# Performance work log

Measured on AMD Instinct MI355X. Metric: run time of the kernel, lower is better.

The kernel has to match this reference:

```python
import jax, jax.numpy as jnp
import numpy as np

HIDDEN = 2048
INTER = 768
NUM_EXPERTS = 32
TOP_K = 4
NUM_TOKENS = 2048


def setup_inputs() -> dict:
    key = jax.random.key(0)
    ks = jax.random.split(key, 5)
    scale = 0.02
    x = jax.random.normal(ks[0], (NUM_TOKENS, HIDDEN), dtype=jnp.float32)
    w_router = jax.random.normal(ks[1], (HIDDEN, NUM_EXPERTS), dtype=jnp.float32) * scale
    w_gate = jax.random.normal(ks[2], (NUM_EXPERTS, HIDDEN, INTER), dtype=jnp.float32) * scale
    w_up = jax.random.normal(ks[3], (NUM_EXPERTS, HIDDEN, INTER), dtype=jnp.float32) * scale
    w_down = jax.random.normal(ks[4], (NUM_EXPERTS, INTER, HIDDEN), dtype=jnp.float32) * scale
    return {"hidden_states": x, "w_router": w_router, "w_gate": w_gate,
            "w_up": w_up, "w_down": w_down}


def reference(hidden_states, w_router, w_gate, w_up, w_down):
    x = hidden_states  # [T, H]
    T = x.shape[0]
    # Router: softmax over experts (in input dtype), top-k, renormalize.
    router_logits = x @ w_router                      # [T, E]
    routing_weights = jax.nn.softmax(router_logits, axis=-1)
    top_w, top_idx = jax.lax.top_k(routing_weights, TOP_K)  # [T, K]
    top_w = top_w / jnp.sum(top_w, axis=-1, keepdims=True)   # norm_topk_prob
    # Dense combine weights: combine[t, e] = routing weight if expert e selected
    # for token t, else 0.  (top-k indices are unique per token.)
    combine = jnp.zeros((T, NUM_EXPERTS), dtype=x.dtype)
    combine = combine.at[jnp.arange(T)[:, None], top_idx].add(top_w)  # [T, E]

    # Scan over experts: each step computes one expert's SwiGLU MLP on all
    # tokens and accumulates it weighted by its combine weight (tokens with
    # zero weight contribute nothing, matching the gather/scatter original).
    def body(acc, expert):
        wg, wu, wd, cw = expert  # [H,I], [H,I], [I,H], [T]
        h = jax.nn.silu(x @ wg) * (x @ wu)   # [T, I]
        return acc + (h @ wd) * cw[:, None], None

    out, _ = jax.lax.scan(body, jnp.zeros_like(x),
                          (w_gate, w_up, w_down, combine.T))
    return out
```

## Files before the change

kernel.cpp:

```cpp
#include <hip/hip_runtime.h>

#define T_TOK 2048
#define HID   2048
#define INTER 768
#define NE    32
#define NSLOT 8192
#define MAXT  96

typedef short bf16x8 __attribute__((ext_vector_type(8)));
typedef float f32x4  __attribute__((ext_vector_type(4)));

__device__ __forceinline__ unsigned short f2b(float f){
  unsigned u = __builtin_bit_cast(unsigned, f);
  u += 0x7fffu + ((u >> 16) & 1u);
  return (unsigned short)(u >> 16);
}
__device__ __forceinline__ unsigned pk2(float a, float b){
  return (unsigned)f2b(a) | ((unsigned)f2b(b) << 16);
}

#define XB_OFF    0ul
#define HBUF_OFF  8388608ul
#define TKW_OFF   20971520ul
#define TKI_OFF   21004288ul
#define ROWS_OFF  21037056ul
#define WTS_OFF   21069824ul
#define OFFS_OFF  21102592ul
#define LOGIT_OFF 21102848ul
#define CNT_OFF   21364992ul
#define FILL_OFF  21365120ul
#define TLIST_OFF 21365248ul
#define T2S_OFF   21365760ul
#define HB2_OFF   21398528ul
#define WS_NEED   (HB2_OFF + 67108864ul)
#define ZERO_OFF  21102848ul
#define ZERO_SZ   (262144ul + 128ul + 128ul)

__global__ void convert_x_kernel(const float* __restrict__ x, ushort* __restrict__ xb){
  int i = (blockIdx.x * 256 + threadIdx.x) * 8;
  float4 a = *(const float4*)(x + i);
  float4 b = *(const float4*)(x + i + 4);
  uint4 o;
  o.x = pk2(a.x, a.y);
  o.y = pk2(a.z, a.w);
  o.z = pk2(b.x, b.y);
  o.w = pk2(b.z, b.w);
  *(uint4*)(xb + i) = o;
}

__global__ void router_gemm(const float* __restrict__ x, const float* __restrict__ wr,
                            float* __restrict__ logits){
  const int tt = blockIdx.x;
  const int kb = blockIdx.y;
  __shared__ float xs[64 * 64];
  __shared__ float wsm[64 * 32];
  const int tid = threadIdx.x;
  const int r = tid >> 5, e = tid & 31;
  float acc[8];
#pragma unroll
  for (int i = 0; i < 8; i++) acc[i] = 0.0f;

  for (int sub = 0; sub < 4; ++sub){
    const int k0 = kb * 256 + sub * 64;
    __syncthreads();
#pragma unroll
    for (int j = 0; j < 4; j++){
      int f4 = tid + j * 256;
      int row = f4 >> 4, c4 = f4 & 15;
      float4 v = *(const float4*)(x + (size_t)(tt * 64 + row) * HID + k0 + c4 * 4);
      *(float4*)(xs + row * 64 + c4 * 4) = v;
    }
#pragma unroll
    for (int j = 0; j < 2; j++){
      int f4 = tid + j * 256;
      int row = f4 >> 3, c4 = f4 & 7;
      float4 v = *(const float4*)(wr + (size_t)(k0 + row) * NE + c4 * 4);
      *(float4*)(wsm + row * NE + c4 * 4) = v;
    }
    __syncthreads();
    for (int kk = 0; kk < 64; kk++){
      float wv = wsm[kk * NE + e];
#pragma unroll
      for (int i = 0; i < 8; i++) acc[i] += xs[(r + i * 8) * 64 + kk] * wv;
    }
  }
#pragma unroll
  for (int i = 0; i < 8; i++)
    atomicAdd(&logits[(size_t)(tt * 64 + r + i * 8) * NE + e], acc[i]);
}

__global__ void topk_kernel(const float* __restrict__ logits, float* __restrict__ topk_w,
                            int* __restrict__ topk_i, int* __restrict__ counts){
  int t = blockIdx.x * blockDim.x + threadIdx.x;
  if (t >= T_TOK) return;
  float l[32];
  const float4* lp = (const float4*)(logits + (size_t)t * NE);
#pragma unroll
  for (int i = 0; i < 8; i++){
    float4 v = lp[i];
    l[i*4+0] = v.x; l[i*4+1] = v.y; l[i*4+2] = v.z; l[i*4+3] = v.w;
  }
  float m = l[0];
#pragma unroll
  for (int i = 1; i < 32; i++) m = fmaxf(m, l[i]);
#pragma unroll
  for (int i = 0; i < 32; i++) l[i] = __expf(l[i] - m);
  float wsel[4]; int isel[4];
#pragma unroll
  for (int k = 0; k < 4; k++){
    float best = l[0]; int bi = 0;
#pragma unroll
    for (int i = 1; i < 32; i++){ if (l[i] > best){ best = l[i]; bi = i; } }
    wsel[k] = best; isel[k] = bi; l[bi] = -1.0f;
  }
  float s4 = wsel[0] + wsel[1] + wsel[2] + wsel[3];
  float inv = 1.0f / s4;
#pragma unroll
  for (int k = 0; k < 4; k++){
    topk_w[t * 4 + k] = wsel[k] * inv;
    topk_i[t * 4 + k] = isel[k];
    atomicAdd(&counts[isel[k]], 1);
  }
}

__global__ void prefix_kernel(const int* __restrict__ counts, int* __restrict__ offsets,
                              int* __restrict__ tlist){
  if (threadIdx.x == 0){
    int a = 0; offsets[0] = 0; int nt_ = 0;
    for (int e = 0; e < NE; e++){
      int c = counts[e];
      for (int m = 0; m * 128 < c && nt_ < MAXT; m++) tlist[nt_++] = e | (m << 16);
      a += c; offsets[e + 1] = a;
    }
    for (; nt_ < MAXT; nt_++) tlist[nt_] = -1;
  }
}

__global__ void scatter_kernel(const int* __restrict__ topk_i, const float* __restrict__ topk_w,
                               const int* __restrict__ offsets, int* __restrict__ fill,
                               int* __restrict__ rows, float* __restrict__ wts,
                               int* __restrict__ t2s){
  int gid = blockIdx.x * 256 + threadIdx.x;
  int t = gid >> 2;
  int e = topk_i[gid];
  int pos = atomicAdd(&fill[e], 1);
  int s = offsets[e] + pos;
  rows[s] = t;
  wts[s] = topk_w[gid];
  t2s[gid] = s;
}

#define NT_GU 32
__global__ __launch_bounds__(512) void gateup_kernel(
    const ushort* __restrict__ xb, const float* __restrict__ wg,
    const float* __restrict__ wu, const int* __restrict__ rows,
    const float* __restrict__ wts, const int* __restrict__ counts,
    const int* __restrict__ offsets, const int* __restrict__ tlist,
    ushort* __restrict__ hbuf)
{
  const int w = tlist[blockIdx.y];
  if (w < 0) return;
  const int e = w & 0xffff, mt = w >> 16;
  const int nt = blockIdx.x;
  const int cnt = counts[e];
  const int off = offsets[e];
  const int n0 = nt * 64;

  __shared__ __align__(16) ushort lds[2 * 16384];

  const int tid = threadIdx.x;

  const int ra = tid >> 2, quad = tid & 3;
  const int srow = mt * 128 + ra;
  const int slotA = off + (srow < cnt ? srow : 0);
  const int tokA = rows[slotA];
  const ushort* agp = xb + (size_t)tokA * HID;
  const int q0 = quad * 2, q1 = q0 + 1;
  const int axk = ra & 7;
  const int adst0 = ra * 64 + (q0 ^ axk) * 8;
  const int adst1 = ra * 64 + (q1 ^ axk) * 8;

  const int bn = tid & 63, kg = tid >> 6;
  const size_t wofs = (size_t)e * (HID * INTER) + n0 + bn;
  const float* wgp = wg + wofs;
  const float* wup = wu + wofs;
  const int bdst = bn * 64 + (kg ^ (bn & 7)) * 8;

  const int lane = tid & 63, wv = tid >> 6;
  const int wm = wv >> 1, wn = wv & 1;
  const int fr = lane & 15, ko = lane >> 4;
  const int fxk = fr & 7;

  f32x4 accg[2][2], accu[2][2];
#pragma unroll
  for (int i = 0; i < 2; i++)
#pragma unroll
    for (int j = 0; j < 2; j++){ accg[i][j] = (f32x4)(0.0f); accu[i][j] = (f32x4)(0.0f); }

  uint4 A0a, A0b, A1a, A1b;
  float G0[8], U0[8], G1[8], U1[8];

  auto loadSet = [&](int k0, uint4 &aa, uint4 &ab, float *g, float *u){
    aa = *(const uint4*)(agp + k0 + q0 * 8);
    ab = *(const uint4*)(agp + k0 + q1 * 8);
    const float* pg_ = wgp + (size_t)(k0 + kg * 8) * INTER;
    const float* pu_ = wup + (size_t)(k0 + kg * 8) * INTER;
#pragma unroll
    for (int kk = 0; kk < 8; kk++){ g[kk] = pg_[(size_t)kk * INTER]; u[kk] = pu_[(size_t)kk * INTER]; }
  };
  auto writeSet = [&](int base, uint4 aa, uint4 ab, const float *g, const float *u){
    ushort* dA = lds + base;
    *(uint4*)(dA + adst0) = aa;
    *(uint4*)(dA + adst1) = ab;
    uint4 pg, pu;
    pg.x = pk2(g[0], g[1]); pg.y = pk2(g[2], g[3]);
    pg.z = pk2(g[4], g[5]); pg.w = pk2(g[6], g[7]);
    pu.x = pk2(u[0], u[1]); pu.y = pk2(u[2], u[3]);
    pu.z = pk2(u[4], u[5]); pu.w = pk2(u[6], u[7]);
    *(uint4*)(dA + 8192 + bdst) = pg;
    *(uint4*)(dA + 12288 + bdst) = pu;
  };
  auto computeTile = [&](int base){
    const ushort* A  = lds + base;
    const ushort* BG = lds + base + 8192;
    const ushort* BU = lds + base + 12288;
#pragma unroll
    for (int kk = 0; kk < 2; kk++){
      const int bsel = ((kk * 4 + ko) ^ fxk) * 8;
      bf16x8 a[2], bg2[2], bu2[2];
#pragma unroll
      for (int mf = 0; mf < 2; mf++)
        a[mf] = *(const bf16x8*)(A + (wm * 32 + mf * 16 + fr) * 64 + bsel);
#pragma unroll
      for (int nf = 0; nf < 2; nf++){
        bg2[nf] = *(const bf16x8*)(BG + (wn * 32 + nf * 16 + fr) * 64 + bsel);
        bu2[nf] = *(const bf16x8*)(BU + (wn * 32 + nf * 16 + fr) * 64 + bsel);
      }
#pragma unroll
      for (int mf = 0; mf < 2; mf++)
#pragma unroll
        for (int nf = 0; nf < 2; nf++){
          accg[mf][nf] = __builtin_amdgcn_mfma_f32_16x16x32_bf16(a[mf], bg2[nf], accg[mf][nf], 0, 0, 0);
          accu[mf][nf] = __builtin_amdgcn_mfma_f32_16x16x32_bf16(a[mf], bu2[nf], accu[mf][nf], 0, 0, 0);
        }
    }
  };

  loadSet(0,  A0a, A0b, G0, U0);
  loadSet(64, A1a, A1b, G1, U1);
  writeSet(0, A0a, A0b, G0, U0);
  __syncthreads();

  for (int t = 0; t < NT_GU; t += 2){
    if (t + 2 < NT_GU) loadSet((t + 2) * 64, A0a, A0b, G0, U0);
    computeTile(0);
    writeSet(16384, A1a, A1b, G1, U1);
    __syncthreads();
    if (t + 3 < NT_GU) loadSet((t + 3) * 64, A1a, A1b, G1, U1);
    computeTile(16384);
    if (t + 2 < NT_GU) writeSet(0, A0a, A0b, G0, U0);
    __syncthreads();
  }

#pragma unroll
  for (int mf = 0; mf < 2; mf++)
#pragma unroll
    for (int j = 0; j < 4; j++){
      int rl = wm * 32 + mf * 16 + ko * 4 + j;
      int gr = mt * 128 + rl;
      if (gr < cnt){
        float w2 = wts[off + gr];
        size_t robase = (size_t)(off + gr) * INTER + n0;
#pragma unroll
        for (int nf = 0; nf < 2; nf++){
          float g = accg[mf][nf][j], u = accu[mf][nf][j];
          float h = (g / (1.0f + __expf(-g))) * u * w2;
          hbuf[robase + wn * 32 + nf * 16 + fr] = f2b(h);
        }
      }
    }
}

#define NT_DN 12
template<bool SLOT>
__global__ __launch_bounds__(512) void down_kernel(
    const ushort* __restrict__ hbuf, const float* __restrict__ wd,
    const int* __restrict__ rows, const int* __restrict__ counts,
    const int* __restrict__ offsets, const int* __restrict__ tlist,
    float* __restrict__ outp)
{
  const int w = tlist[blockIdx.y];
  if (w < 0) return;
  const int e = w & 0xffff, mt = w >> 16;
  const int nt = blockIdx.x;
  const int cnt = counts[e];
  const int off = offsets[e];
  const int n0 = nt * 64;

  __shared__ __align__(16) ushort lds[2 * 12288];

  const int tid = threadIdx.x;

  const int ra = tid >> 2, quad = tid & 3;
  const int srow = mt * 128 + ra;
  const int slotA = off + (srow < cnt ? srow : 0);
  const ushort* agp = hbuf + (size_t)slotA * INTER;
  const int q0 = quad * 2, q1 = q0 + 1;
  const int axk = ra & 7;
  const int adst0 = ra * 64 + (q0 ^ axk) * 8;
  const int adst1 = ra * 64 + (q1 ^ axk) * 8;

  const int bn = tid & 63, kg = tid >> 6;
  const float* wdp = wd + (size_t)e * (INTER * HID) + n0 + bn;
  const int bdst = bn * 64 + (kg ^ (bn & 7)) * 8;

  const int lane = tid & 63, wv = tid >> 6;
  const int wm = wv >> 1, wn = wv & 1;
  const int fr = lane & 15, ko = lane >> 4;
  const int fxk = fr & 7;

  f32x4 acc[2][2];
#pragma unroll
  for (int i = 0; i < 2; i++)
#pragma unroll
    for (int j = 0; j < 2; j++) acc[i][j] = (f32x4)(0.0f);

  uint4 A0a, A0b, A1a, A1b;
  float B0[8], B1[8];

  auto loadSet = [&](int k0, uint4 &aa, uint4 &ab, float *b){
    aa = *(const uint4*)(agp + k0 + q0 * 8);
    ab = *(const uint4*)(agp + k0 + q1 * 8);
    const float* p = wdp + (size_t)(k0 + kg * 8) * HID;
#pragma unroll
    for (int kk = 0; kk < 8; kk++) b[kk] = p[(size_t)kk * HID];
  };
  auto writeSet = [&](int base, uint4 aa, uint4 ab, const float *b){
    ushort* dA = lds + base;
    *(uint4*)(dA + adst0) = aa;
    *(uint4*)(dA + adst1) = ab;
    uint4 pb;
    pb.x = pk2(b[0], b[1]); pb.y = pk2(b[2], b[3]);
    pb.z = pk2(b[4], b[5]); pb.w = pk2(b[6], b[7]);
    *(uint4*)(dA + 8192 + bdst) = pb;
  };
  auto computeTile = [&](int base){
    const ushort* A = lds + base;
    const ushort* B = lds + base + 8192;
#pragma unroll
    for (int kk = 0; kk < 2; kk++){
      const int bsel = ((kk * 4 + ko) ^ fxk) * 8;
      bf16x8 a[2], b2[2];
#pragma unroll
      for (int mf = 0; mf < 2; mf++)
        a[mf] = *(const bf16x8*)(A + (wm * 32 + mf * 16 + fr) * 64 + bsel);
#pragma unroll
      for (int nf = 0; nf < 2; nf++)
        b2[nf] = *(const bf16x8*)(B + (wn * 32 + nf * 16 + fr) * 64 + bsel);
#pragma unroll
      for (int mf = 0; mf < 2; mf++)
#pragma unroll
        for (int nf = 0; nf < 2; nf++)
          acc[mf][nf] = __builtin_amdgcn_mfma_f32_16x16x32_bf16(a[mf], b2[nf], acc[mf][nf], 0, 0, 0);
    }
  };

  loadSet(0,  A0a, A0b, B0);
  loadSet(64, A1a, A1b, B1);
  writeSet(0, A0a, A0b, B0);
  __syncthreads();

  for (int t = 0; t < NT_DN; t += 2){
    if (t + 2 < NT_DN) loadSet((t + 2) * 64, A0a, A0b, B0);
    computeTile(0);
    writeSet(12288, A1a, A1b, B1);
    __syncthreads();
    if (t + 3 < NT_DN) loadSet((t + 3) * 64, A1a, A1b, B1);
    computeTile(12288);
    if (t + 2 < NT_DN) writeSet(0, A0a, A0b, B0);
    __syncthreads();
  }

#pragma unroll
  for (int mf = 0; mf < 2; mf++)
#pragma unroll
    for (int j = 0; j < 4; j++){
      int rl = wm * 32 + mf * 16 + ko * 4 + j;
      int gr = mt * 128 + rl;
      if (gr < cnt){
        if (SLOT){
          float* obase = outp + (size_t)(off + gr) * HID + n0;
#pragma unroll
          for (int nf = 0; nf < 2; nf++)
            obase[wn * 32 + nf * 16 + fr] = acc[mf][nf][j];
        } else {
          int tok = rows[off + gr];
          float* obase = outp + (size_t)tok * HID + n0;
#pragma unroll
          for (int nf = 0; nf < 2; nf++)
            atomicAdd(obase + wn * 32 + nf * 16 + fr, acc[mf][nf][j]);
        }
      }
    }
}

__global__ void combine_kernel(const float* __restrict__ hbuf2, const int* __restrict__ t2s,
                               float* __restrict__ out){
  const int t = blockIdx.y;
  const int c4 = (blockIdx.x * 256 + threadIdx.x) * 4;
  const int s0 = t2s[t * 4 + 0], s1 = t2s[t * 4 + 1];
  const int s2 = t2s[t * 4 + 2], s3 = t2s[t * 4 + 3];
  float4 a = *(const float4*)(hbuf2 + (size_t)s0 * HID + c4);
  float4 b = *(const float4*)(hbuf2 + (size_t)s1 * HID + c4);
  float4 c = *(const float4*)(hbuf2 + (size_t)s2 * HID + c4);
  float4 d = *(const float4*)(hbuf2 + (size_t)s3 * HID + c4);
  float4 r;
  r.x = a.x + b.x + c.x + d.x;
  r.y = a.y + b.y + c.y + d.y;
  r.z = a.z + b.z + c.z + d.z;
  r.w = a.w + b.w + c.w + d.w;
  *(float4*)(out + (size_t)t * HID + c4) = r;
}

extern "C" void kernel_launch(void* const* d_in, const int* in_sizes, int n_in,
                              void* d_out, int out_size, void* d_ws, size_t ws_size,
                              hipStream_t stream){
  const float* x  = (const float*)d_in[0];
  const float* wr = (const float*)d_in[1];
  const float* wg = (const float*)d_in[2];
  const float* wu = (const float*)d_in[3];
  const float* wd = (const float*)d_in[4];
  float* out = (float*)d_out;
  char* ws = (char*)d_ws;

  ushort* xb     = (ushort*)(ws + XB_OFF);
  ushort* hbuf   = (ushort*)(ws + HBUF_OFF);
  float*  topkw  = (float*)(ws + TKW_OFF);
  int*    topki  = (int*)(ws + TKI_OFF);
  int*    rows   = (int*)(ws + ROWS_OFF);
  float*  wts    = (float*)(ws + WTS_OFF);
  int*    offs   = (int*)(ws + OFFS_OFF);
  float*  logits = (float*)(ws + LOGIT_OFF);
  int*    counts = (int*)(ws + CNT_OFF);
  int*    fill   = (int*)(ws + FILL_OFF);
  int*    tlist  = (int*)(ws + TLIST_OFF);
  int*    t2s    = (int*)(ws + T2S_OFF);
  float*  hbuf2  = (float*)(ws + HB2_OFF);

  const bool slotpath = (ws_size >= WS_NEED);

  hipMemsetAsync(ws + ZERO_OFF, 0, ZERO_SZ, stream);

  convert_x_kernel<<<2048, 256, 0, stream>>>(x, xb);
  router_gemm<<<dim3(32, 8), 256, 0, stream>>>(x, wr, logits);
  topk_kernel<<<8, 256, 0, stream>>>(logits, topkw, topki, counts);
  prefix_kernel<<<1, 64, 0, stream>>>(counts, offs, tlist);
  scatter_kernel<<<32, 256, 0, stream>>>(topki, topkw, offs, fill, rows, wts, t2s);
  gateup_kernel<<<dim3(12, MAXT), 512, 0, stream>>>(xb, wg, wu, rows, wts, counts, offs, tlist, hbuf);
  if (slotpath){
    down_kernel<true><<<dim3(32, MAXT), 512, 0, stream>>>(hbuf, wd, rows, counts, offs, tlist, hbuf2);
    combine_kernel<<<dim3(2, T_TOK), 256, 0, stream>>>(hbuf2, t2s, out);
  } else {
    hipMemsetAsync(d_out, 0, (size_t)out_size * sizeof(float), stream);
    down_kernel<false><<<dim3(32, MAXT), 512, 0, stream>>>(hbuf, wd, rows, counts, offs, tlist, out);
  }
}
```

Before: 348.0 us.

## Widen N tiles and switch to padded LDS with K=32 steps in MoE GEMMs

Both the gate/up and down grouped GEMM kernels now use wider output tiles: 128 columns for gate/up and 256 for down, where both were 64 before. Each tile is paired with a shallower K step of 32. The XOR-swizzled LDS layout is replaced by a row stride padded to 40 elements. The aim is more reuse of the A tile (tokens) per block, with fewer blocks re-reading activations and less total fp32 weight traffic per block. In exchange there are fewer blocks and more accumulator registers per thread, so occupancy and latency hiding may drop, and the loop now runs twice as many iterations with one barrier each.

```diff
diff --git a/kernel.cpp b/kernel.cpp
--- a/kernel.cpp
+++ b/kernel.cpp
@@ -150,7 +150,8 @@
   t2s[gid] = s;
 }
 
-#define NT_GU 32
+#define NT_GU 64
+#define GU_STRIDE 15360
 __global__ __launch_bounds__(512) void gateup_kernel(
     const ushort* __restrict__ xb, const float* __restrict__ wg,
     const float* __restrict__ wu, const int* __restrict__ rows,
@@ -164,102 +165,88 @@
   const int nt = blockIdx.x;
   const int cnt = counts[e];
   const int off = offsets[e];
-  const int n0 = nt * 64;
-
-  __shared__ __align__(16) ushort lds[2 * 16384];
+  const int n0 = nt * 128;
+
+  __shared__ __align__(16) ushort lds[2 * GU_STRIDE];
 
   const int tid = threadIdx.x;
 
-  const int ra = tid >> 2, quad = tid & 3;
-  const int srow = mt * 128 + ra;
-  const int slotA = off + (srow < cnt ? srow : 0);
-  const int tokA = rows[slotA];
-  const ushort* agp = xb + (size_t)tokA * HID;
-  const int q0 = quad * 2, q1 = q0 + 1;
-  const int axk = ra & 7;
-  const int adst0 = ra * 64 + (q0 ^ axk) * 8;
-  const int adst1 = ra * 64 + (q1 ^ axk) * 8;
-
-  const int bn = tid & 63, kg = tid >> 6;
-  const size_t wofs = (size_t)e * (HID * INTER) + n0 + bn;
+  const int arow = tid >> 2, ablk = tid & 3;
+  const int srow = mt * 128 + arow;
+  const int tokA = rows[off + (srow < cnt ? srow : 0)];
+  const ushort* agp = xb + (size_t)tokA * HID + ablk * 8;
+  const int adst = arow * 40 + ablk * 8;
+
+  const int bcol = tid & 127, bkg = tid >> 7;
+  const size_t wofs = (size_t)e * (HID * INTER) + (size_t)bkg * 8 * INTER + n0 + bcol;
   const float* wgp = wg + wofs;
   const float* wup = wu + wofs;
-  const int bdst = bn * 64 + (kg ^ (bn & 7)) * 8;
+  const int bdst = bcol * 40 + bkg * 8;
 
   const int lane = tid & 63, wv = tid >> 6;
   const int wm = wv >> 1, wn = wv & 1;
   const int fr = lane & 15, ko = lane >> 4;
-  const int fxk = fr & 7;
-
-  f32x4 accg[2][2], accu[2][2];
+
+  f32x4 accg[2][4], accu[2][4];
 #pragma unroll
   for (int i = 0; i < 2; i++)
 #pragma unroll
-    for (int j = 0; j < 2; j++){ accg[i][j] = (f32x4)(0.0f); accu[i][j] = (f32x4)(0.0f); }
-
-  uint4 A0a, A0b, A1a, A1b;
-  float G0[8], U0[8], G1[8], U1[8];
-
-  auto loadSet = [&](int k0, uint4 &aa, uint4 &ab, float *g, float *u){
-    aa = *(const uint4*)(agp + k0 + q0 * 8);
-    ab = *(const uint4*)(agp + k0 + q1 * 8);
-    const float* pg_ = wgp + (size_t)(k0 + kg * 8) * INTER;
-    const float* pu_ = wup + (size_t)(k0 + kg * 8) * INTER;
-#pragma unroll
-    for (int kk = 0; kk < 8; kk++){ g[kk] = pg_[(size_t)kk * INTER]; u[kk] = pu_[(size_t)kk * INTER]; }
-  };
-  auto writeSet = [&](int base, uint4 aa, uint4 ab, const float *g, const float *u){
-    ushort* dA = lds + base;
-    *(uint4*)(dA + adst0) = aa;
-    *(uint4*)(dA + adst1) = ab;
+    for (int j = 0; j < 4; j++){ accg[i][j] = (f32x4)(0.0f); accu[i][j] = (f32x4)(0.0f); }
+
+  uint4 pa;
+  float sg[8], su[8];
+
+  auto loadSet = [&](int k0){
+    pa = *(const uint4*)(agp + k0);
+    const float* pg_ = wgp + (size_t)k0 * INTER;
+    const float* pu_ = wup + (size_t)k0 * INTER;
+#pragma unroll
+    for (int kk = 0; kk < 8; kk++){ sg[kk] = pg_[(size_t)kk * INTER]; su[kk] = pu_[(size_t)kk * INTER]; }
+  };
+  auto writeSet = [&](int base){
+    *(uint4*)(lds + base + adst) = pa;
     uint4 pg, pu;
-    pg.x = pk2(g[0], g[1]); pg.y = pk2(g[2], g[3]);
-    pg.z = pk2(g[4], g[5]); pg.w = pk2(g[6], g[7]);
-    pu.x = pk2(u[0], u[1]); pu.y = pk2(u[2], u[3]);
-    pu.z = pk2(u[4], u[5]); pu.w = pk2(u[6], u[7]);
-    *(uint4*)(dA + 8192 + bdst) = pg;
-    *(uint4*)(dA + 12288 + bdst) = pu;
+    pg.x = pk2(sg[0], sg[1]); pg.y = pk2(sg[2], sg[3]);
+    pg.z = pk2(sg[4], sg[5]); pg.w = pk2(sg[6], sg[7]);
+    pu.x = pk2(su[0], su[1]); pu.y = pk2(su[2], su[3]);
+    pu.z = pk2(su[4], su[5]); pu.w = pk2(su[6], su[7]);
+    *(uint4*)(lds + base + 5120 + bdst)  = pg;
+    *(uint4*)(lds + base + 10240 + bdst) = pu;
   };
   auto computeTile = [&](int base){
     const ushort* A  = lds + base;
-    const ushort* BG = lds + base + 8192;
-    const ushort* BU = lds + base + 12288;
-#pragma unroll
-    for (int kk = 0; kk < 2; kk++){
-      const int bsel = ((kk * 4 + ko) ^ fxk) * 8;
-      bf16x8 a[2], bg2[2], bu2[2];
-#pragma unroll
-      for (int mf = 0; mf < 2; mf++)
-        a[mf] = *(const bf16x8*)(A + (wm * 32 + mf * 16 + fr) * 64 + bsel);
-#pragma unroll
-      for (int nf = 0; nf < 2; nf++){
-        bg2[nf] = *(const bf16x8*)(BG + (wn * 32 + nf * 16 + fr) * 64 + bsel);
-        bu2[nf] = *(const bf16x8*)(BU + (wn * 32 + nf * 16 + fr) * 64 + bsel);
+    const ushort* BG = lds + base + 5120;
+    const ushort* BU = lds + base + 10240;
+    bf16x8 a[2], bg2[4], bu2[4];
+#pragma unroll
+    for (int mf = 0; mf < 2; mf++)
+      a[mf] = *(const bf16x8*)(A + (wm * 32 + mf * 16 + fr) * 40 + ko * 8);
+#pragma unroll
+    for (int nf = 0; nf < 4; nf++){
+      bg2[nf] = *(const bf16x8*)(BG + (wn * 64 + nf * 16 + fr) * 40 + ko * 8);
+      bu2[nf] = *(const bf16x8*)(BU + (wn * 64 + nf * 16 + fr) * 40 + ko * 8);
+    }
+#pragma unroll
+    for (int mf = 0; mf < 2; mf++)
+#pragma unroll
+      for (int nf = 0; nf < 4; nf++){
+        accg[mf][nf] = __builtin_amdgcn_mfma_f32_16x16x32_bf16(a[mf], bg2[nf], accg[mf][nf], 0, 0, 0);
+        accu[mf][nf] = __builtin_amdgcn_mfma_f32_16x16x32_bf16(a[mf], bu2[nf], accu[mf][nf], 0, 0, 0);
       }
-#pragma unroll
-      for (int mf = 0; mf < 2; mf++)
-#pragma unroll
-        for (int nf = 0; nf < 2; nf++){
-          accg[mf][nf] = __builtin_amdgcn_mfma_f32_16x16x32_bf16(a[mf], bg2[nf], accg[mf][nf], 0, 0, 0);
-          accu[mf][nf] = __builtin_amdgcn_mfma_f32_16x16x32_bf16(a[mf], bu2[nf], accu[mf][nf], 0, 0, 0);
-        }
-    }
-  };
-
-  loadSet(0,  A0a, A0b, G0, U0);
-  loadSet(64, A1a, A1b, G1, U1);
-  writeSet(0, A0a, A0b, G0, U0);
+  };
+
+  loadSet(0);
+  writeSet(0);
   __syncthreads();
 
-  for (int t = 0; t < NT_GU; t += 2){
-    if (t + 2 < NT_GU) loadSet((t + 2) * 64, A0a, A0b, G0, U0);
-    computeTile(0);
-    writeSet(16384, A1a, A1b, G1, U1);
+  int cbase = 0;
+  for (int t = 0; t < NT_GU; ++t){
+    const int nb = cbase ^ GU_STRIDE;
+    if (t + 1 < NT_GU) loadSet((t + 1) * 32);
+    computeTile(cbase);
+    if (t + 1 < NT_GU) writeSet(nb);
     __syncthreads();
-    if (t + 3 < NT_GU) loadSet((t + 3) * 64, A1a, A1b, G1, U1);
-    computeTile(16384);
-    if (t + 2 < NT_GU) writeSet(0, A0a, A0b, G0, U0);
-    __syncthreads();
+    cbase = nb;
   }
 
 #pragma unroll
@@ -272,16 +259,17 @@
         float w2 = wts[off + gr];
         size_t robase = (size_t)(off + gr) * INTER + n0;
 #pragma unroll
-        for (int nf = 0; nf < 2; nf++){
+        for (int nf = 0; nf < 4; nf++){
           float g = accg[mf][nf][j], u = accu[mf][nf][j];
           float h = (g / (1.0f + __expf(-g))) * u * w2;
-          hbuf[robase + wn * 32 + nf * 16 + fr] = f2b(h);
+          hbuf[robase + wn * 64 + nf * 16 + fr] = f2b(h);
         }
       }
     }
 }
 
-#define NT_DN 12
+#define NT_DN 24
+#define DN_STRIDE 15360
 template<bool SLOT>
 __global__ __launch_bounds__(512) void down_kernel(
     const ushort* __restrict__ hbuf, const float* __restrict__ wd,
@@ -295,110 +283,100 @@
   const int nt = blockIdx.x;
   const int cnt = counts[e];
   const int off = offsets[e];
-  const int n0 = nt * 64;
-
-  __shared__ __align__(16) ushort lds[2 * 12288];
+  const int n0 = nt * 256;
+
+  __shared__ __align__(16) ushort lds[2 * DN_STRIDE];
 
   const int tid = threadIdx.x;
 
-  const int ra = tid >> 2, quad = tid & 3;
-  const int srow = mt * 128 + ra;
+  const int arow = tid >> 2, ablk = tid & 3;
+  const int srow = mt * 128 + arow;
   const int slotA = off + (srow < cnt ? srow : 0);
-  const ushort* agp = hbuf + (size_t)slotA * INTER;
-  const int q0 = quad * 2, q1 = q0 + 1;
-  const int axk = ra & 7;
-  const int adst0 = ra * 64 + (q0 ^ axk) * 8;
-  const int adst1 = ra * 64 + (q1 ^ axk) * 8;
-
-  const int bn = tid & 63, kg = tid >> 6;
-  const float* wdp = wd + (size_t)e * (INTER * HID) + n0 + bn;
-  const int bdst = bn * 64 + (kg ^ (bn & 7)) * 8;
+  const ushort* agp = hbuf + (size_t)slotA * INTER + ablk * 8;
+  const int adst = arow * 40 + ablk * 8;
+
+  const int bcol = tid & 255, bkg = tid >> 8;
+  const float* wdp = wd + (size_t)e * (INTER * HID) + (size_t)bkg * 16 * HID + n0 + bcol;
+  const int bdst = 5120 + bcol * 40 + bkg * 16;
 
   const int lane = tid & 63, wv = tid >> 6;
-  const int wm = wv >> 1, wn = wv & 1;
+  const int wm = wv >> 2, wn = wv & 3;
   const int fr = lane & 15, ko = lane >> 4;
-  const int fxk = fr & 7;
-
-  f32x4 acc[2][2];
-#pragma unroll
-  for (int i = 0; i < 2; i++)
-#pragma unroll
-    for (int j = 0; j < 2; j++) acc[i][j] = (f32x4)(0.0f);
-
-  uint4 A0a, A0b, A1a, A1b;
-  float B0[8], B1[8];
-
-  auto loadSet = [&](int k0, uint4 &aa, uint4 &ab, float *b){
-    aa = *(const uint4*)(agp + k0 + q0 * 8);
-    ab = *(const uint4*)(agp + k0 + q1 * 8);
-    const float* p = wdp + (size_t)(k0 + kg * 8) * HID;
-#pragma unroll
-    for (int kk = 0; kk < 8; kk++) b[kk] = p[(size_t)kk * HID];
-  };
-  auto writeSet = [&](int base, uint4 aa, uint4 ab, const float *b){
-    ushort* dA = lds + base;
-    *(uint4*)(dA + adst0) = aa;
-    *(uint4*)(dA + adst1) = ab;
-    uint4 pb;
-    pb.x = pk2(b[0], b[1]); pb.y = pk2(b[2], b[3]);
-    pb.z = pk2(b[4], b[5]); pb.w = pk2(b[6], b[7]);
-    *(uint4*)(dA + 8192 + bdst) = pb;
+
+  f32x4 acc[4][4];
+#pragma unroll
+  for (int i = 0; i < 4; i++)
+#pragma unroll
+    for (int j = 0; j < 4; j++) acc[i][j] = (f32x4)(0.0f);
+
+  uint4 pa;
+  float sb[16];
+
+  auto loadSet = [&](int k0){
+    pa = *(const uint4*)(agp + k0);
+    const float* p = wdp + (size_t)k0 * HID;
+#pragma unroll
+    for (int kk = 0; kk < 16; kk++) sb[kk] = p[(size_t)kk * HID];
+  };
+  auto writeSet = [&](int base){
+    *(uint4*)(lds + base + adst) = pa;
+    uint4 p0, p1;
+    p0.x = pk2(sb[0], sb[1]);  p0.y = pk2(sb[2], sb[3]);
+    p0.z = pk2(sb[4], sb[5]);  p0.w = pk2(sb[6], sb[7]);
+    p1.x = pk2(sb[8], sb[9]);  p1.y = pk2(sb[10], sb[11]);
+    p1.z = pk2(sb[12], sb[13]); p1.w = pk2(sb[14], sb[15]);
+    *(uint4*)(lds + base + bdst)     = p0;
+    *(uint4*)(lds + base + bdst + 8) = p1;
   };
   auto computeTile = [&](int base){
     const ushort* A = lds + base;
-    const ushort* B = lds + base + 8192;
-#pragma unroll
-    for (int kk = 0; kk < 2; kk++){
-      const int bsel = ((kk * 4 + ko) ^ fxk) * 8;
-      bf16x8 a[2], b2[2];
-#pragma unroll
-      for (int mf = 0; mf < 2; mf++)
-        a[mf] = *(const bf16x8*)(A + (wm * 32 + mf * 16 + fr) * 64 + bsel);
-#pragma unroll
-      for (int nf = 0; nf < 2; nf++)
-        b2[nf] = *(const bf16x8*)(B + (wn * 32 + nf * 16 + fr) * 64 + bsel);
-#pragma unroll
-      for (int mf = 0; mf < 2; mf++)
-#pragma unroll
-        for (int nf = 0; nf < 2; nf++)
-          acc[mf][nf] = __builtin_amdgcn_mfma_f32_16x16x32_bf16(a[mf], b2[nf], acc[mf][nf], 0, 0, 0);
-    }
-  };
-
-  loadSet(0,  A0a, A0b, B0);
-  loadSet(64, A1a, A1b, B1);
-  writeSet(0, A0a, A0b, B0);
+    const ushort* B = lds + base + 5120;
+    bf16x8 a[4], b2[4];
+#pragma unroll
+    for (int mf = 0; mf < 4; mf++)
+      a[mf] = *(const bf16x8*)(A + (wm * 64 + mf * 16 + fr) * 40 + ko * 8);
+#pragma unroll
+    for (int nf = 0; nf < 4; nf++)
+      b2[nf] = *(const bf16x8*)(B + (wn * 64 + nf * 16 + fr) * 40 + ko * 8);
+#pragma unroll
+    for (int mf = 0; mf < 4; mf++)
+#pragma unroll
+      for (int nf = 0; nf < 4; nf++)
+        acc[mf][nf] = __builtin_amdgcn_mfma_f32_16x16x32_bf16(a[mf], b2[nf], acc[mf][nf], 0, 0, 0);
+  };
+
+  loadSet(0);
+  writeSet(0);
   __syncthreads();
 
-  for (int t = 0; t < NT_DN; t += 2){
-    if (t + 2 < NT_DN) loadSet((t + 2) * 64, A0a, A0b, B0);
-    computeTile(0);
-    writeSet(12288, A1a, A1b, B1);
+  int cbase = 0;
+  for (int t = 0; t < NT_DN; ++t){
+    const int nb = cbase ^ DN_STRIDE;
+    if (t + 1 < NT_DN) loadSet((t + 1) * 32);
+    computeTile(cbase);
+    if (t + 1 < NT_DN) writeSet(nb);
     __syncthreads();
-    if (t + 3 < NT_DN) loadSet((t + 3) * 64, A1a, A1b, B1);
-    computeTile(12288);
-    if (t + 2 < NT_DN) writeSet(0, A0a, A0b, B0);
-    __syncthreads();
-  }
-
-#pragma unroll
-  for (int mf = 0; mf < 2; mf++)
+    cbase = nb;
+  }
+
+#pragma unroll
+  for (int mf = 0; mf < 4; mf++)
 #pragma unroll
     for (int j = 0; j < 4; j++){
-      int rl = wm * 32 + mf * 16 + ko * 4 + j;
+      int rl = wm * 64 + mf * 16 + ko * 4 + j;
       int gr = mt * 128 + rl;
       if (gr < cnt){
         if (SLOT){
           float* obase = outp + (size_t)(off + gr) * HID + n0;
 #pragma unroll
-          for (int nf = 0; nf < 2; nf++)
-            obase[wn * 32 + nf * 16 + fr] = acc[mf][nf][j];
+          for (int nf = 0; nf < 4; nf++)
+            obase[wn * 64 + nf * 16 + fr] = acc[mf][nf][j];
         } else {
           int tok = rows[off + gr];
           float* obase = outp + (size_t)tok * HID + n0;
 #pragma unroll
-          for (int nf = 0; nf < 2; nf++)
-            atomicAdd(obase + wn * 32 + nf * 16 + fr, acc[mf][nf][j]);
+          for (int nf = 0; nf < 4; nf++)
+            atomicAdd(obase + wn * 64 + nf * 16 + fr, acc[mf][nf][j]);
         }
       }
     }
@@ -456,12 +434,12 @@
   topk_kernel<<<8, 256, 0, stream>>>(logits, topkw, topki, counts);
   prefix_kernel<<<1, 64, 0, stream>>>(counts, offs, tlist);
   scatter_kernel<<<32, 256, 0, stream>>>(topki, topkw, offs, fill, rows, wts, t2s);
-  gateup_kernel<<<dim3(12, MAXT), 512, 0, stream>>>(xb, wg, wu, rows, wts, counts, offs, tlist, hbuf);
+  gateup_kernel<<<dim3(6, MAXT), 512, 0, stream>>>(xb, wg, wu, rows, wts, counts, offs, tlist, hbuf);
   if (slotpath){
-    down_kernel<true><<<dim3(32, MAXT), 512, 0, stream>>>(hbuf, wd, rows, counts, offs, tlist, hbuf2);
+    down_kernel<true><<<dim3(8, MAXT), 512, 0, stream>>>(hbuf, wd, rows, counts, offs, tlist, hbuf2);
     combine_kernel<<<dim3(2, T_TOK), 256, 0, stream>>>(hbuf2, t2s, out);
   } else {
     hipMemsetAsync(d_out, 0, (size_t)out_size * sizeof(float), stream);
-    down_kernel<false><<<dim3(32, MAXT), 512, 0, stream>>>(hbuf, wd, rows, counts, offs, tlist, out);
-  }
-}
+    down_kernel<false><<<dim3(8, MAXT), 512, 0, stream>>>(hbuf, wd, rows, counts, offs, tlist, out);
+  }
+}
```

Measured after the change: 425.7 us. 1.22x slower.

## Stage A tiles via global_load_lds with smaller K tiles and higher occupancy

Applied to the files above, without the earlier changes.

The gate/up and down kernels now copy the bf16 activation tile straight from global memory into LDS with the global_load_lds builtin, bypassing registers. K tiles shrink from 64 to 32, which halves the LDS footprint and register staging, and launch bounds now request more resident blocks per CU. The swizzle layout is reworked to match the 32-wide tiles. In exchange, twice as many iterations and __syncthreads calls are needed, and correctness depends on the builtin writing to the expected per-lane LDS layout.

```diff
diff --git a/kernel.cpp b/kernel.cpp
--- a/kernel.cpp
+++ b/kernel.cpp
@@ -10,6 +10,15 @@
 typedef short bf16x8 __attribute__((ext_vector_type(8)));
 typedef float f32x4  __attribute__((ext_vector_type(4)));
 
+#if defined(__has_builtin)
+#  if __has_builtin(__builtin_amdgcn_global_load_lds)
+#    define HAS_GLDS 1
+#  endif
+#endif
+#ifndef HAS_GLDS
+#  define HAS_GLDS 0
+#endif
+
 __device__ __forceinline__ unsigned short f2b(float f){
   unsigned u = __builtin_bit_cast(unsigned, f);
   u += 0x7fffu + ((u >> 16) & 1u);
@@ -17,6 +26,16 @@
 }
 __device__ __forceinline__ unsigned pk2(float a, float b){
   return (unsigned)f2b(a) | ((unsigned)f2b(b) << 16);
+}
+
+__device__ __forceinline__ void stageA16(const ushort* gsrc, ushort* ldst){
+#if HAS_GLDS
+  __builtin_amdgcn_global_load_lds(
+      (const __attribute__((address_space(1))) unsigned int*)gsrc,
+      (__attribute__((address_space(3))) unsigned int*)ldst, 16, 0, 0);
+#else
+  *(uint4*)ldst = *(const uint4*)gsrc;
+#endif
 }
 
 #define XB_OFF    0ul
@@ -150,8 +169,9 @@
   t2s[gid] = s;
 }
 
-#define NT_GU 32
-__global__ __launch_bounds__(512) void gateup_kernel(
+#define NT_GU 64
+#define GU_BUF 8192
+__global__ __launch_bounds__(512, 6) void gateup_kernel(
     const ushort* __restrict__ xb, const float* __restrict__ wg,
     const float* __restrict__ wu, const int* __restrict__ rows,
     const float* __restrict__ wts, const int* __restrict__ counts,
@@ -166,30 +186,37 @@
   const int off = offsets[e];
   const int n0 = nt * 64;
 
-  __shared__ __align__(16) ushort lds[2 * 16384];
+  __shared__ __align__(16) ushort lds[2 * GU_BUF];
 
   const int tid = threadIdx.x;
 
-  const int ra = tid >> 2, quad = tid & 3;
-  const int srow = mt * 128 + ra;
-  const int slotA = off + (srow < cnt ? srow : 0);
-  const int tokA = rows[slotA];
-  const ushort* agp = xb + (size_t)tokA * HID;
-  const int q0 = quad * 2, q1 = q0 + 1;
-  const int axk = ra & 7;
-  const int adst0 = ra * 64 + (q0 ^ axk) * 8;
-  const int adst1 = ra * 64 + (q1 ^ axk) * 8;
+  const int ar = tid >> 2, adc = tid & 3;
+  const int alc = adc ^ ((ar >> 1) & 3);
+  const int srow = mt * 128 + ar;
+  const int tokA = rows[off + (srow < cnt ? srow : 0)];
+  const ushort* agp = xb + (size_t)tokA * HID + alc * 8;
 
   const int bn = tid & 63, kg = tid >> 6;
-  const size_t wofs = (size_t)e * (HID * INTER) + n0 + bn;
+  const size_t wofs = (size_t)e * (HID * INTER) + (size_t)(kg * 4) * INTER + n0 + bn;
   const float* wgp = wg + wofs;
   const float* wup = wu + wofs;
-  const int bdst = bn * 64 + (kg ^ (bn & 7)) * 8;
+  const int bofs = bn * 32 + ((kg >> 1) ^ ((bn >> 1) & 3)) * 8 + (kg & 1) * 4;
 
   const int lane = tid & 63, wv = tid >> 6;
   const int wm = wv >> 1, wn = wv & 1;
   const int fr = lane & 15, ko = lane >> 4;
-  const int fxk = fr & 7;
+
+  int aoff[2], boff[2];
+#pragma unroll
+  for (int mf = 0; mf < 2; mf++){
+    int r = wm * 32 + mf * 16 + fr;
+    aoff[mf] = r * 32 + ((ko ^ ((r >> 1) & 3)) * 8);
+  }
+#pragma unroll
+  for (int nf = 0; nf < 2; nf++){
+    int c = wn * 32 + nf * 16 + fr;
+    boff[nf] = c * 32 + ((ko ^ ((c >> 1) & 3)) * 8);
+  }
 
   f32x4 accg[2][2], accu[2][2];
 #pragma unroll
@@ -197,69 +224,55 @@
 #pragma unroll
     for (int j = 0; j < 2; j++){ accg[i][j] = (f32x4)(0.0f); accu[i][j] = (f32x4)(0.0f); }
 
-  uint4 A0a, A0b, A1a, A1b;
-  float G0[8], U0[8], G1[8], U1[8];
-
-  auto loadSet = [&](int k0, uint4 &aa, uint4 &ab, float *g, float *u){
-    aa = *(const uint4*)(agp + k0 + q0 * 8);
-    ab = *(const uint4*)(agp + k0 + q1 * 8);
-    const float* pg_ = wgp + (size_t)(k0 + kg * 8) * INTER;
-    const float* pu_ = wup + (size_t)(k0 + kg * 8) * INTER;
-#pragma unroll
-    for (int kk = 0; kk < 8; kk++){ g[kk] = pg_[(size_t)kk * INTER]; u[kk] = pu_[(size_t)kk * INTER]; }
-  };
-  auto writeSet = [&](int base, uint4 aa, uint4 ab, const float *g, const float *u){
-    ushort* dA = lds + base;
-    *(uint4*)(dA + adst0) = aa;
-    *(uint4*)(dA + adst1) = ab;
-    uint4 pg, pu;
-    pg.x = pk2(g[0], g[1]); pg.y = pk2(g[2], g[3]);
-    pg.z = pk2(g[4], g[5]); pg.w = pk2(g[6], g[7]);
-    pu.x = pk2(u[0], u[1]); pu.y = pk2(u[2], u[3]);
-    pu.z = pk2(u[4], u[5]); pu.w = pk2(u[6], u[7]);
-    *(uint4*)(dA + 8192 + bdst) = pg;
-    *(uint4*)(dA + 12288 + bdst) = pu;
+  float sg[4], su[4];
+
+  auto loadB = [&](int k0){
+    const float* pg_ = wgp + (size_t)k0 * INTER;
+    const float* pu_ = wup + (size_t)k0 * INTER;
+#pragma unroll
+    for (int kk = 0; kk < 4; kk++){ sg[kk] = pg_[(size_t)kk * INTER]; su[kk] = pu_[(size_t)kk * INTER]; }
+  };
+  auto writeB = [&](int base){
+    uint2 pg, pu;
+    pg.x = pk2(sg[0], sg[1]); pg.y = pk2(sg[2], sg[3]);
+    pu.x = pk2(su[0], su[1]); pu.y = pk2(su[2], su[3]);
+    *(uint2*)(lds + base + 4096 + bofs) = pg;
+    *(uint2*)(lds + base + 6144 + bofs) = pu;
   };
   auto computeTile = [&](int base){
-    const ushort* A  = lds + base;
-    const ushort* BG = lds + base + 8192;
-    const ushort* BU = lds + base + 12288;
-#pragma unroll
-    for (int kk = 0; kk < 2; kk++){
-      const int bsel = ((kk * 4 + ko) ^ fxk) * 8;
-      bf16x8 a[2], bg2[2], bu2[2];
-#pragma unroll
-      for (int mf = 0; mf < 2; mf++)
-        a[mf] = *(const bf16x8*)(A + (wm * 32 + mf * 16 + fr) * 64 + bsel);
+    bf16x8 a[2], bg2[2], bu2[2];
+#pragma unroll
+    for (int mf = 0; mf < 2; mf++) a[mf] = *(const bf16x8*)(lds + base + aoff[mf]);
+#pragma unroll
+    for (int nf = 0; nf < 2; nf++){
+      bg2[nf] = *(const bf16x8*)(lds + base + 4096 + boff[nf]);
+      bu2[nf] = *(const bf16x8*)(lds + base + 6144 + boff[nf]);
+    }
+#pragma unroll
+    for (int mf = 0; mf < 2; mf++)
 #pragma unroll
       for (int nf = 0; nf < 2; nf++){
-        bg2[nf] = *(const bf16x8*)(BG + (wn * 32 + nf * 16 + fr) * 64 + bsel);
-        bu2[nf] = *(const bf16x8*)(BU + (wn * 32 + nf * 16 + fr) * 64 + bsel);
+        accg[mf][nf] = __builtin_amdgcn_mfma_f32_16x16x32_bf16(a[mf], bg2[nf], accg[mf][nf], 0, 0, 0);
+        accu[mf][nf] = __builtin_amdgcn_mfma_f32_16x16x32_bf16(a[mf], bu2[nf], accu[mf][nf], 0, 0, 0);
       }
-#pragma unroll
-      for (int mf = 0; mf < 2; mf++)
-#pragma unroll
-        for (int nf = 0; nf < 2; nf++){
-          accg[mf][nf] = __builtin_amdgcn_mfma_f32_16x16x32_bf16(a[mf], bg2[nf], accg[mf][nf], 0, 0, 0);
-          accu[mf][nf] = __builtin_amdgcn_mfma_f32_16x16x32_bf16(a[mf], bu2[nf], accu[mf][nf], 0, 0, 0);
-        }
-    }
-  };
-
-  loadSet(0,  A0a, A0b, G0, U0);
-  loadSet(64, A1a, A1b, G1, U1);
-  writeSet(0, A0a, A0b, G0, U0);
+  };
+
+  stageA16(agp, lds + tid * 8);
+  loadB(0);
+  writeB(0);
   __syncthreads();
 
-  for (int t = 0; t < NT_GU; t += 2){
-    if (t + 2 < NT_GU) loadSet((t + 2) * 64, A0a, A0b, G0, U0);
-    computeTile(0);
-    writeSet(16384, A1a, A1b, G1, U1);
+  int cb = 0;
+  for (int t = 0; t < NT_GU; ++t){
+    const int nb = cb ^ GU_BUF;
+    if (t + 1 < NT_GU){
+      stageA16(agp + (t + 1) * 32, lds + nb + tid * 8);
+      loadB((t + 1) * 32);
+    }
+    computeTile(cb);
+    if (t + 1 < NT_GU) writeB(nb);
     __syncthreads();
-    if (t + 3 < NT_GU) loadSet((t + 3) * 64, A1a, A1b, G1, U1);
-    computeTile(16384);
-    if (t + 2 < NT_GU) writeSet(0, A0a, A0b, G0, U0);
-    __syncthreads();
+    cb = nb;
   }
 
 #pragma unroll
@@ -281,9 +294,10 @@
     }
 }
 
-#define NT_DN 12
+#define NT_DN 24
+#define DN_BUF 6144
 template<bool SLOT>
-__global__ __launch_bounds__(512) void down_kernel(
+__global__ __launch_bounds__(512, 6) void down_kernel(
     const ushort* __restrict__ hbuf, const float* __restrict__ wd,
     const int* __restrict__ rows, const int* __restrict__ counts,
     const int* __restrict__ offsets, const int* __restrict__ tlist,
@@ -297,27 +311,35 @@
   const int off = offsets[e];
   const int n0 = nt * 64;
 
-  __shared__ __align__(16) ushort lds[2 * 12288];
+  __shared__ __align__(16) ushort lds[2 * DN_BUF];
 
   const int tid = threadIdx.x;
 
-  const int ra = tid >> 2, quad = tid & 3;
-  const int srow = mt * 128 + ra;
+  const int ar = tid >> 2, adc = tid & 3;
+  const int alc = adc ^ ((ar >> 1) & 3);
+  const int srow = mt * 128 + ar;
   const int slotA = off + (srow < cnt ? srow : 0);
-  const ushort* agp = hbuf + (size_t)slotA * INTER;
-  const int q0 = quad * 2, q1 = q0 + 1;
-  const int axk = ra & 7;
-  const int adst0 = ra * 64 + (q0 ^ axk) * 8;
-  const int adst1 = ra * 64 + (q1 ^ axk) * 8;
+  const ushort* agp = hbuf + (size_t)slotA * INTER + alc * 8;
 
   const int bn = tid & 63, kg = tid >> 6;
-  const float* wdp = wd + (size_t)e * (INTER * HID) + n0 + bn;
-  const int bdst = bn * 64 + (kg ^ (bn & 7)) * 8;
+  const float* wdp = wd + (size_t)e * (INTER * HID) + (size_t)(kg * 4) * HID + n0 + bn;
+  const int bofs = bn * 32 + ((kg >> 1) ^ ((bn >> 1) & 3)) * 8 + (kg & 1) * 4;
 
   const int lane = tid & 63, wv = tid >> 6;
   const int wm = wv >> 1, wn = wv & 1;
   const int fr = lane & 15, ko = lane >> 4;
-  const int fxk = fr & 7;
+
+  int aoff[2], boff[2];
+#pragma unroll
+  for (int mf = 0; mf < 2; mf++){
+    int r = wm * 32 + mf * 16 + fr;
+    aoff[mf] = r * 32 + ((ko ^ ((r >> 1) & 3)) * 8);
+  }
+#pragma unroll
+  for (int nf = 0; nf < 2; nf++){
+    int c = wn * 32 + nf * 16 + fr;
+    boff[nf] = c * 32 + ((ko ^ ((c >> 1) & 3)) * 8);
+  }
 
   f32x4 acc[2][2];
 #pragma unroll
@@ -325,60 +347,47 @@
 #pragma unroll
     for (int j = 0; j < 2; j++) acc[i][j] = (f32x4)(0.0f);
 
-  uint4 A0a, A0b, A1a, A1b;
-  float B0[8], B1[8];
-
-  auto loadSet = [&](int k0, uint4 &aa, uint4 &ab, float *b){
-    aa = *(const uint4*)(agp + k0 + q0 * 8);
-    ab = *(const uint4*)(agp + k0 + q1 * 8);
-    const float* p = wdp + (size_t)(k0 + kg * 8) * HID;
-#pragma unroll
-    for (int kk = 0; kk < 8; kk++) b[kk] = p[(size_t)kk * HID];
-  };
-  auto writeSet = [&](int base, uint4 aa, uint4 ab, const float *b){
-    ushort* dA = lds + base;
-    *(uint4*)(dA + adst0) = aa;
-    *(uint4*)(dA + adst1) = ab;
-    uint4 pb;
-    pb.x = pk2(b[0], b[1]); pb.y = pk2(b[2], b[3]);
-    pb.z = pk2(b[4], b[5]); pb.w = pk2(b[6], b[7]);
-    *(uint4*)(dA + 8192 + bdst) = pb;
+  float sb[4];
+
+  auto loadB = [&](int k0){
+    const float* p = wdp + (size_t)k0 * HID;
+#pragma unroll
+    for (int kk = 0; kk < 4; kk++) sb[kk] = p[(size_t)kk * HID];
+  };
+  auto writeB = [&](int base){
+    uint2 pb;
+    pb.x = pk2(sb[0], sb[1]); pb.y = pk2(sb[2], sb[3]);
+    *(uint2*)(lds + base + 4096 + bofs) = pb;
   };
   auto computeTile = [&](int base){
-    const ushort* A = lds + base;
-    const ushort* B = lds + base + 8192;
-#pragma unroll
-    for (int kk = 0; kk < 2; kk++){
-      const int bsel = ((kk * 4 + ko) ^ fxk) * 8;
-      bf16x8 a[2], b2[2];
-#pragma unroll
-      for (int mf = 0; mf < 2; mf++)
-        a[mf] = *(const bf16x8*)(A + (wm * 32 + mf * 16 + fr) * 64 + bsel);
+    bf16x8 a[2], b2[2];
+#pragma unroll
+    for (int mf = 0; mf < 2; mf++) a[mf] = *(const bf16x8*)(lds + base + aoff[mf]);
+#pragma unroll
+    for (int nf = 0; nf < 2; nf++) b2[nf] = *(const bf16x8*)(lds + base + 4096 + boff[nf]);
+#pragma unroll
+    for (int mf = 0; mf < 2; mf++)
 #pragma unroll
       for (int nf = 0; nf < 2; nf++)
-        b2[nf] = *(const bf16x8*)(B + (wn * 32 + nf * 16 + fr) * 64 + bsel);
-#pragma unroll
-      for (int mf = 0; mf < 2; mf++)
-#pragma unroll
-        for (int nf = 0; nf < 2; nf++)
-          acc[mf][nf] = __builtin_amdgcn_mfma_f32_16x16x32_bf16(a[mf], b2[nf], acc[mf][nf], 0, 0, 0);
-    }
-  };
-
-  loadSet(0,  A0a, A0b, B0);
-  loadSet(64, A1a, A1b, B1);
-  writeSet(0, A0a, A0b, B0);
+        acc[mf][nf] = __builtin_amdgcn_mfma_f32_16x16x32_bf16(a[mf], b2[nf], acc[mf][nf], 0, 0, 0);
+  };
+
+  stageA16(agp, lds + tid * 8);
+  loadB(0);
+  writeB(0);
   __syncthreads();
 
-  for (int t = 0; t < NT_DN; t += 2){
-    if (t + 2 < NT_DN) loadSet((t + 2) * 64, A0a, A0b, B0);
-    computeTile(0);
-    writeSet(12288, A1a, A1b, B1);
+  int cb = 0;
+  for (int t = 0; t < NT_DN; ++t){
+    const int nb = cb ^ DN_BUF;
+    if (t + 1 < NT_DN){
+      stageA16(agp + (t + 1) * 32, lds + nb + tid * 8);
+      loadB((t + 1) * 32);
+    }
+    computeTile(cb);
+    if (t + 1 < NT_DN) writeB(nb);
     __syncthreads();
-    if (t + 3 < NT_DN) loadSet((t + 3) * 64, A1a, A1b, B1);
-    computeTile(12288);
-    if (t + 2 < NT_DN) writeSet(0, A0a, A0b, B0);
-    __syncthreads();
+    cb = nb;
   }
 
 #pragma unroll
```

Result: slower. 365.0 us (+4.9%).
